# Kernel optimization log

Hardware: AMD Instinct MI355X
Metric: run time of the kernel (lower is better)

## Reference

```python
import jax, jax.numpy as jnp
import numpy as np

# Mega (Flash-Quad) encoder layer: MultiHeadEMA + moving-average gated chunked attention + ScaleNorm
L, B, D = 2048, 16, 512        # seq_len, batch, embed_dim (fairseq L,B,D layout)
H, Z, NDIM = 1024, 128, 2      # hdim, zdim, EMA ndim
CHUNK = 128                    # Flash-Quad chunk size
MAXPOS = 1024                  # SimpleRelativePositionalBias max positions
EPS = 1e-6                     # ScaleNorm eps


def setup_inputs() -> dict:
    key = jax.random.key(0)
    ks = jax.random.split(key, 16)
    def nrm(k, shape, s=0.02):
        return jax.random.normal(k, shape, jnp.float32) * s
    return dict(
        x=jax.random.normal(ks[0], (L, B, D), jnp.float32),
        # MultiHeadEMA params (bidirectional -> kernel_dim = 2*D)
        ema_delta=nrm(ks[1], (2 * D, NDIM, 1), 1.0),
        ema_alpha=nrm(ks[2], (2 * D, NDIM, 1), 1.0),
        ema_beta=nrm(ks[3], (2 * D, NDIM, 1), 0.02),
        ema_gamma=nrm(ks[4], (2 * D, NDIM), 1.0),
        ema_omega=nrm(ks[5], (D,), 1.0),
        # projections
        Wv=nrm(ks[6], (D, H)), bv=jnp.zeros((H,), jnp.float32),
        Wmx=nrm(ks[7], (D, Z + H + 2 * D)), bmx=jnp.zeros((Z + H + 2 * D,), jnp.float32),
        Wh=nrm(ks[8], (H, D)), bh=jnp.zeros((D,), jnp.float32),
        # per-dim q/k affine (gamma/beta) on shared z
        qk_gamma=nrm(ks[9], (2, Z), 0.1) + 1.0,
        qk_beta=nrm(ks[10], (2, Z), 0.1),
        # simple relative positional bias over chunk length
        rel_pos_bias=nrm(ks[11], (2 * MAXPOS - 1,), 0.02),
        # ScaleNorm scalar
        norm_scalar=jnp.ones((), jnp.float32),
    )


def _ema(x, delta, alpha, beta, gamma, omega):
    """Bidirectional multi-dim damped EMA via FFT convolution. x: (L,B,D) -> (L,B,D)."""
    Lx, Bx, Dx = x.shape
    residual = x * omega
    xt = jnp.transpose(x, (1, 2, 0))                      # B,D,L
    p = jax.nn.sigmoid(delta)                             # 2D,n,1
    q = 1.0 - p * jax.nn.sigmoid(alpha)                   # 2D,n,1 in (0,1)
    vander = jnp.arange(Lx, dtype=jnp.float32)[None, None, :] * jnp.log(q)  # 2D,n,L
    kern = jnp.einsum('dnl,dn->dl', (p * beta) * jnp.exp(vander),
                      gamma * (1.0 / np.sqrt(NDIM)))      # 2D,L
    k1, k2 = kern[:Dx], kern[Dx:]
    # combined causal + anticausal kernel of length 2L-1, input left-padded by L-1
    kc = jnp.pad(k1, ((0, 0), (Lx - 1, 0))) + jnp.pad(k2[:, ::-1], ((0, 0), (0, Lx - 1)))
    xp = jnp.pad(xt, ((0, 0), (0, 0), (Lx - 1, 0)))
    n = 2 * (2 * Lx - 1)
    out = jnp.fft.irfft(jnp.fft.rfft(xp, n=n) * jnp.fft.rfft(kc, n=n), n=n)
    out = out[..., 2 * Lx - 2: 2 * Lx - 2 + Lx]           # B,D,L
    return jax.nn.silu(jnp.transpose(out, (2, 0, 1)) + residual)


def _forward(x, ema_delta, ema_alpha, ema_beta, ema_gamma, ema_omega,
             Wv, bv, Wmx, bmx, Wh, bh, qk_gamma, qk_beta, rel_pos_bias, norm_scalar):
    Lx, Bx, Dx = x.shape
    residual = x
    v = jax.nn.silu(x @ Wv + bv)                          # L,B,H
    mx = _ema(x, ema_delta, ema_alpha, ema_beta, ema_gamma, ema_omega)  # L,B,D
    base = mx @ Wmx + bmx                                 # L,B,D+Z+H+D
    u = jax.nn.sigmoid(base[..., :Dx])                    # update gate
    zr = jax.nn.silu(base[..., Dx:Dx + Z + H])
    hx = base[..., Dx + Z + H:]
    z, r = zr[..., :Z], zr[..., Z:]                       # shared z, reset gate r
    zqk = z[..., None, :] * qk_gamma + qk_beta            # L,B,2,Z
    nc = Lx // CHUNK
    q = jnp.transpose(zqk[..., 0, :], (1, 0, 2)).reshape(Bx, nc, CHUNK, Z)
    k = jnp.transpose(zqk[..., 1, :], (1, 0, 2)).reshape(Bx, nc, CHUNK, Z)
    vc = jnp.transpose(v, (1, 0, 2)).reshape(Bx, nc, CHUNK, H)
    # Toeplitz relative bias: bias[i,j] = rel_pos_bias[MAXPOS-1 + j - i]
    idx = (MAXPOS - 1) + jnp.arange(CHUNK)[None, :] - jnp.arange(CHUNK)[:, None]
    bias = rel_pos_bias[idx]                              # C,C
    qk = jnp.einsum('bnqz,bnkz->bnqk', q * (Z ** -0.5), k) + bias
    attn = jax.nn.softmax(qk, axis=-1)                    # B,nc,C,C
    h = jnp.einsum('bnqk,bnkh->bnqh', attn, vc).reshape(Bx, Lx, H)
    h = jnp.transpose(h, (1, 0, 2))                       # L,B,H
    h = jax.nn.silu(hx + (h * r) @ Wh + bh)               # L,B,D
    out = residual + u * (h - residual)                   # addcmul gated residual
    ms = jnp.mean(out * out, axis=-1, keepdims=True)      # ScaleNorm
    out = norm_scalar * out * jax.lax.rsqrt(ms + EPS)
    return out, attn


def reference(x, ema_delta, ema_alpha, ema_beta, ema_gamma, ema_omega,
              Wv, bv, Wmx, bmx, Wh, bh, qk_gamma, qk_beta, rel_pos_bias, norm_scalar):
    return _forward(x, ema_delta, ema_alpha, ema_beta, ema_gamma, ema_omega,
                    Wv, bv, Wmx, bmx, Wh, bh, qk_gamma, qk_beta, rel_pos_bias, norm_scalar)
```

## Files before the change

### kernel.cpp

```cpp
#include <hip/hip_runtime.h>
#include <math.h>

#define L_DIM 2048
#define B_DIM 16
#define D_DIM 512
#define H_DIM 1024
#define Z_DIM 128
#define NC    16
#define BASE_N 2176
#define ROWS  (L_DIM*B_DIM)
#define NSEG  32
#define SLEN  64
#define CHAINS 8192

typedef unsigned short bf16_t;
typedef __attribute__((ext_vector_type(8))) short short8;
typedef __attribute__((ext_vector_type(4))) float f32x4;

__device__ __forceinline__ float sigmoidf_(float x){ return 1.f/(1.f+__expf(-x)); }
__device__ __forceinline__ float siluf_(float x){ return x/(1.f+__expf(-x)); }
__device__ __forceinline__ float fbits(unsigned int b){ union{unsigned int i; float f;} c; c.i=b; return c.f; }
__device__ __forceinline__ unsigned short f2bf(float f){
  union{float f; unsigned int i;} c; c.f=f;
  unsigned int r = c.i + 0x7FFFu + ((c.i>>16)&1u);
  return (unsigned short)(r>>16);
}
__device__ __forceinline__ float bf2f(unsigned short u){ return fbits(((unsigned int)u)<<16); }

__device__ __forceinline__ void load8(const float* __restrict__ p, float* d){
  float4 a = *(const float4*)p; float4 b = *(const float4*)(p+4);
  d[0]=a.x; d[1]=a.y; d[2]=a.z; d[3]=a.w; d[4]=b.x; d[5]=b.y; d[6]=b.z; d[7]=b.w;
}
__device__ __forceinline__ void load8(const bf16_t* __restrict__ p, float* d){
  uint4 u = *(const uint4*)p;
  d[0]=fbits(u.x<<16); d[1]=fbits(u.x&0xFFFF0000u);
  d[2]=fbits(u.y<<16); d[3]=fbits(u.y&0xFFFF0000u);
  d[4]=fbits(u.z<<16); d[5]=fbits(u.z&0xFFFF0000u);
  d[6]=fbits(u.w<<16); d[7]=fbits(u.w&0xFFFF0000u);
}
__device__ __forceinline__ void store8bf(bf16_t* p, const float* v){
  uint4 s;
  s.x = (unsigned int)f2bf(v[0]) | ((unsigned int)f2bf(v[1])<<16);
  s.y = (unsigned int)f2bf(v[2]) | ((unsigned int)f2bf(v[3])<<16);
  s.z = (unsigned int)f2bf(v[4]) | ((unsigned int)f2bf(v[5])<<16);
  s.w = (unsigned int)f2bf(v[6]) | ((unsigned int)f2bf(v[7])<<16);
  *(uint4*)p = s;
}

__device__ __forceinline__ void glds16(const void* g, void* l) {
  __builtin_amdgcn_global_load_lds(
      (const __attribute__((address_space(1))) unsigned int*)g,
      (__attribute__((address_space(3))) unsigned int*)l, 16, 0, 0);
}

__global__ __launch_bounds__(256) void transpose_all_kernel(
    const float* __restrict__ Wv, const float* __restrict__ Wmx,
    const float* __restrict__ Wh, bf16_t* __restrict__ Wvt,
    bf16_t* __restrict__ Wmxt, bf16_t* __restrict__ Wht)
{
  __shared__ float t[32][33];
  int blk = blockIdx.x;
  const float* W; bf16_t* Wt; int K, N, bx, by;
  if (blk < 512)       { W=Wv;  Wt=Wvt;  K=512;  N=1024; bx=blk&31;  by=blk>>5; }
  else if (blk < 1600) { blk-=512;  W=Wmx; Wt=Wmxt; K=512;  N=2176; bx=blk%68; by=blk/68; }
  else                 { blk-=1600; W=Wh;  Wt=Wht;  K=1024; N=512;  bx=blk&15; by=blk>>4; }
  int lx = threadIdx.x & 31, ly = threadIdx.x >> 5;
  #pragma unroll
  for (int i = 0; i < 32; i += 8)
    t[ly+i][lx] = W[(size_t)(by*32+ly+i)*N + bx*32 + lx];
  __syncthreads();
  #pragma unroll
  for (int i = 0; i < 32; i += 8)
    Wt[(size_t)(bx*32+ly+i)*K + by*32 + lx] = f2bf(t[lx][ly+i]);
}

__global__ __launch_bounds__(256) void ema_carry_kernel(
    const float* __restrict__ x, const float* __restrict__ delta,
    const float* __restrict__ alpha, bf16_t* __restrict__ xb,
    float* __restrict__ carry)
{
  int idx = blockIdx.x*256 + threadIdx.x;
  int d = idx & 511, c = idx & 8191, s = idx >> 13;
  float qf0 = 1.f - sigmoidf_(delta[d*2+0])*sigmoidf_(alpha[d*2+0]);
  float qf1 = 1.f - sigmoidf_(delta[d*2+1])*sigmoidf_(alpha[d*2+1]);
  int dd = d + 512;
  float qb0 = 1.f - sigmoidf_(delta[dd*2+0])*sigmoidf_(alpha[dd*2+0]);
  float qb1 = 1.f - sigmoidf_(delta[dd*2+1])*sigmoidf_(alpha[dd*2+1]);
  size_t off = (size_t)s*SLEN*CHAINS + c;
  float h0=0.f, h1=0.f;
  #pragma unroll
  for (int t = 0; t < SLEN; ++t) {
    size_t a = off + (size_t)t*CHAINS;
    float xv = x[a];
    xb[a] = f2bf(xv);
    h0 = fmaf(qf0, h0, xv); h1 = fmaf(qf1, h1, xv);
  }
  float g0=0.f, g1=0.f;
  #pragma unroll
  for (int t = SLEN-1; t >= 0; --t) {
    float xv = bf2f(xb[off + (size_t)t*CHAINS]);
    g0 = fmaf(qb0, g0, xv); g1 = fmaf(qb1, g1, xv);
  }
  carry[(size_t)s*CHAINS + c]              = h0;
  carry[(size_t)s*CHAINS + c + 262144]     = h1;
  carry[(size_t)s*CHAINS + c + 524288]     = g0;
  carry[(size_t)s*CHAINS + c + 786432]     = g1;
}

__global__ __launch_bounds__(256) void ema_combine_kernel(
    const float* __restrict__ delta, const float* __restrict__ alpha,
    float* __restrict__ carry)
{
  int c = blockIdx.x*256 + threadIdx.x;
  int d = c & 511;
  float qf0 = 1.f - sigmoidf_(delta[d*2+0])*sigmoidf_(alpha[d*2+0]);
  float qf1 = 1.f - sigmoidf_(delta[d*2+1])*sigmoidf_(alpha[d*2+1]);
  int dd = d + 512;
  float qb0 = 1.f - sigmoidf_(delta[dd*2+0])*sigmoidf_(alpha[dd*2+0]);
  float qb1 = 1.f - sigmoidf_(delta[dd*2+1])*sigmoidf_(alpha[dd*2+1]);
  float df0=qf0, df1=qf1, db0=qb0, db1=qb1;
  #pragma unroll
  for (int i = 0; i < 6; ++i) { df0*=df0; df1*=df1; db0*=db0; db1*=db1; }
  float h0=0.f, h1=0.f;
  for (int s = 0; s < NSEG; ++s) {
    size_t a = (size_t)s*CHAINS + c;
    float t0 = carry[a], t1 = carry[a+262144];
    carry[a] = h0; carry[a+262144] = h1;
    h0 = fmaf(df0, h0, t0); h1 = fmaf(df1, h1, t1);
  }
  float g0=0.f, g1=0.f;
  for (int s = NSEG-1; s >= 0; --s) {
    size_t a = (size_t)s*CHAINS + c;
    float t0 = carry[a+524288], t1 = carry[a+786432];
    carry[a+524288] = g0; carry[a+786432] = g1;
    g0 = fmaf(db0, g0, t0); g1 = fmaf(db1, g1, t1);
  }
}

__global__ __launch_bounds__(256) void ema_apply_kernel(
    const bf16_t* __restrict__ xb, const float* __restrict__ delta,
    const float* __restrict__ alpha, const float* __restrict__ beta,
    const float* __restrict__ gamma, const float* __restrict__ omega,
    const float* __restrict__ carry, bf16_t* __restrict__ mx)
{
  int idx = blockIdx.x*256 + threadIdx.x;
  int d = idx & 511, c = idx & 8191, s = idx >> 13;
  const float rs = 0.70710678118654752f;
  float pf0 = sigmoidf_(delta[d*2+0]), pf1 = sigmoidf_(delta[d*2+1]);
  float qf0 = 1.f - pf0*sigmoidf_(alpha[d*2+0]);
  float qf1 = 1.f - pf1*sigmoidf_(alpha[d*2+1]);
  float cf0 = pf0*beta[d*2+0]*gamma[d*2+0]*rs;
  float cf1 = pf1*beta[d*2+1]*gamma[d*2+1]*rs;
  int dd = d + 512;
  float pb0 = sigmoidf_(delta[dd*2+0]), pb1 = sigmoidf_(delta[dd*2+1]);
  float qb0 = 1.f - pb0*sigmoidf_(alpha[dd*2+0]);
  float qb1 = 1.f - pb1*sigmoidf_(alpha[dd*2+1]);
  float cb0 = pb0*beta[dd*2+0]*gamma[dd*2+0]*rs;
  float cb1 = pb1*beta[dd*2+1]*gamma[dd*2+1]*rs;
  float om = omega[d];
  size_t off = (size_t)s*SLEN*CHAINS + c;
  float h0 = carry[(size_t)s*CHAINS + c];
  float h1 = carry[(size_t)s*CHAINS + c + 262144];
  float yv[SLEN];
  #pragma unroll
  for (int t = 0; t < SLEN; ++t) {
    float xv = bf2f(xb[off + (size_t)t*CHAINS]);
    h0 = fmaf(qf0, h0, xv); h1 = fmaf(qf1, h1, xv);
    yv[t] = fmaf(cf0, h0, cf1*h1);
  }
  float g0 = carry[(size_t)s*CHAINS + c + 524288];
  float g1 = carry[(size_t)s*CHAINS + c + 786432];
  #pragma unroll
  for (int t = SLEN-1; t >= 0; --t) {
    size_t a = off + (size_t)t*CHAINS;
    float xv = bf2f(xb[a]);
    g0 = fmaf(qb0, g0, xv); g1 = fmaf(qb1, g1, xv);
    float sv = yv[t] + fmaf(cb0, g0, cb1*g1) + xv*om;
    mx[a] = f2bf(siluf_(sv));
  }
}

#define GEMM_PROLOG(Aptr, Bptr, Kdim)                                        \
  int tid = threadIdx.x;                                                     \
  int wave = tid >> 6, lane = tid & 63;                                      \
  int lrow = lane >> 3, lchunk = ((lane & 7) - lrow) & 7;                    \
  const bf16_t* Ag = (Aptr) + (size_t)(wave*32 + lrow)*(Kdim) + lchunk*8;    \
  const bf16_t* Bg = (Bptr) + (size_t)(wave*32 + lrow)*(Kdim) + lchunk*8;    \
  int wm = wave >> 1, wn = wave & 1;                                         \
  int fr = lane & 15, fq = lane >> 4;                                        \
  f32x4 acc[4][4];                                                           \
  _Pragma("unroll") for (int i = 0; i < 4; ++i)                              \
    _Pragma("unroll") for (int j = 0; j < 4; ++j)                            \
      acc[i][j] = (f32x4){0.f,0.f,0.f,0.f};

#define GEMM_KLOOP(Kdim)                                                     \
  for (int k0 = 0; k0 < (Kdim); k0 += 64) {                                  \
    __syncthreads();                                                         \
    _Pragma("unroll") for (int j = 0; j < 4; ++j) {                          \
      glds16(Ag + (size_t)j*8*(Kdim) + k0, As + (wave*32 + j*8)*64);         \
      glds16(Bg + (size_t)j*8*(Kdim) + k0, Bs + (wave*32 + j*8)*64);         \
    }                                                                        \
    __syncthreads();                                                         \
    _Pragma("unroll") for (int kk = 0; kk < 2; ++kk) {                       \
      short8 af[4], bfr[4];                                                  \
      _Pragma("unroll") for (int mi = 0; mi < 4; ++mi) {                     \
        int R = wm*64 + mi*16 + fr;                                          \
        af[mi] = *(const short8*)&As[R*64 + (((kk<<2)+fq+R)&7)*8];           \
      }                                                                      \
      _Pragma("unroll") for (int ni = 0; ni < 4; ++ni) {                     \
        int R = wn*64 + ni*16 + fr;                                          \
        bfr[ni] = *(const short8*)&Bs[R*64 + (((kk<<2)+fq+R)&7)*8];          \
      }                                                                      \
      _Pragma("unroll") for (int mi = 0; mi < 4; ++mi)                       \
        _Pragma("unroll") for (int ni = 0; ni < 4; ++ni)                     \
          acc[mi][ni] = __builtin_amdgcn_mfma_f32_16x16x32_bf16(             \
              af[mi], bfr[ni], acc[mi][ni], 0, 0, 0);                        \
    }                                                                        \
  }

__global__ __launch_bounds__(256) void mfma_gemm_kernel(
    const bf16_t* __restrict__ A, const bf16_t* __restrict__ Bt,
    const float* __restrict__ bias, const bf16_t* __restrict__ Add, int addLd,
    bf16_t* __restrict__ C, int N, int K, int nT, int act)
{
  __shared__ __align__(16) char smem[34816];
  bf16_t* As = (bf16_t*)smem;
  bf16_t* Bs = (bf16_t*)(smem + 16384);
  bf16_t* Cs = (bf16_t*)smem;
  int flat = blockIdx.x;
  int xcd = flat & 7, g = flat >> 3;
  int mT8 = (int)(gridDim.x / (unsigned)nT) >> 3;
  int mt = xcd*mT8 + g / nT;
  int nt = g % nT;
  int m0 = mt*128, n0 = nt*128;
  GEMM_PROLOG(A + (size_t)m0*K, Bt + (size_t)n0*K, K)
  GEMM_KLOOP(K)
  __syncthreads();
  #pragma unroll
  for (int ni = 0; ni < 4; ++ni) {
    int cl = wn*64 + ni*16 + fr;
    int gn = n0 + cl;
    float bv = bias[gn];
    #pragma unroll
    for (int mi = 0; mi < 4; ++mi) {
      #pragma unroll
      for (int r = 0; r < 4; ++r) {
        int ml = wm*64 + mi*16 + fq*4 + r;
        float val = acc[mi][ni][r] + bv;
        if (Add) val += bf2f(Add[(size_t)(m0+ml)*addLd + gn]);
        if (act == 1) val = siluf_(val);
        Cs[ml*136 + cl] = f2bf(val);
      }
    }
  }
  __syncthreads();
  int row = tid >> 1, c0 = (tid & 1)*64;
  #pragma unroll
  for (int q = 0; q < 8; ++q)
    *(uint4*)(C + (size_t)(m0+row)*N + n0 + c0 + q*8) =
        *(const uint4*)&Cs[row*136 + c0 + q*8];
}

__global__ __launch_bounds__(256) void mfma_gemm_v_kernel(
    const bf16_t* __restrict__ A, const bf16_t* __restrict__ Bt,
    const float* __restrict__ bias, bf16_t* __restrict__ vt, int nT, int K)
{
  __shared__ __align__(16) char smem[34816];
  bf16_t* As = (bf16_t*)smem;
  bf16_t* Bs = (bf16_t*)(smem + 16384);
  bf16_t* Cs = (bf16_t*)smem;
  int flat = blockIdx.x;
  int xcd = flat & 7, g = flat >> 3;
  int mT8 = (int)(gridDim.x / (unsigned)nT) >> 3;
  int mt = xcd*mT8 + g / nT;
  int nt = g % nT;
  int m0 = mt*128, n0 = nt*128;
  GEMM_PROLOG(A + (size_t)m0*K, Bt + (size_t)n0*K, K)
  GEMM_KLOOP(K)
  __syncthreads();
  #pragma unroll
  for (int ni = 0; ni < 4; ++ni) {
    int cl = wn*64 + ni*16 + fr;
    float bv = bias[n0 + cl];
    #pragma unroll
    for (int mi = 0; mi < 4; ++mi) {
      #pragma unroll
      for (int r = 0; r < 4; ++r) {
        int ml = wm*64 + mi*16 + fq*4 + r;
        Cs[ml*136 + cl] = f2bf(siluf_(acc[mi][ni][r] + bv));
      }
    }
  }
  __syncthreads();
  int b = tid >> 4, h0l = (tid & 15)*8;
  int nchunk = mt >> 4, kbase = (mt & 15)*8;
  #pragma unroll
  for (int j = 0; j < 8; ++j) {
    int hl = h0l + j;
    uint4 s;
    s.x = (unsigned int)Cs[(0*16 + b)*136 + hl] |
          ((unsigned int)Cs[(1*16 + b)*136 + hl] << 16);
    s.y = (unsigned int)Cs[(2*16 + b)*136 + hl] |
          ((unsigned int)Cs[(3*16 + b)*136 + hl] << 16);
    s.z = (unsigned int)Cs[(4*16 + b)*136 + hl] |
          ((unsigned int)Cs[(5*16 + b)*136 + hl] << 16);
    s.w = (unsigned int)Cs[(6*16 + b)*136 + hl] |
          ((unsigned int)Cs[(7*16 + b)*136 + hl] << 16);
    *(uint4*)&vt[((size_t)(b*NC + nchunk)*H_DIM + n0 + hl)*128 + kbase] = s;
  }
}

__global__ __launch_bounds__(256) void attn_scores_mfma_kernel(
    const bf16_t* __restrict__ base, const float* __restrict__ qkg,
    const float* __restrict__ qkb, const float* __restrict__ rpb,
    float* __restrict__ attn_out, bf16_t* __restrict__ p_bf)
{
  __shared__ bf16_t qs[128*136];
  __shared__ bf16_t ks[128*136];
  int blk = blockIdx.x;
  int b = blk >> 4, n = blk & 15;
  int tid = threadIdx.x;
  {
    int r = tid >> 1, z0 = (tid & 1)*64;
    size_t rowoff = ((size_t)((n*128 + r)*B_DIM + b))*BASE_N + 512 + z0;
    #pragma unroll
    for (int cchunk = 0; cchunk < 8; ++cchunk) {
      float t8[8], qv[8], kv[8];
      load8(base + rowoff + cchunk*8, t8);
      #pragma unroll
      for (int j = 0; j < 8; ++j) {
        int z = z0 + cchunk*8 + j;
        float zs = siluf_(t8[j]);
        qv[j] = fmaf(zs, qkg[z],     qkb[z]);
        kv[j] = fmaf(zs, qkg[128+z], qkb[128+z]);
      }
      store8bf(&qs[r*136 + z0 + cchunk*8], qv);
      store8bf(&ks[r*136 + z0 + cchunk*8], kv);
    }
  }
  __syncthreads();
  int wave = tid >> 6, lane = tid & 63;
  int fr = lane & 15, fq = lane >> 4;
  f32x4 acc[2][8];
  #pragma unroll
  for (int i = 0; i < 2; ++i)
    #pragma unroll
    for (int j = 0; j < 8; ++j)
      acc[i][j] = (f32x4){0.f,0.f,0.f,0.f};
  #pragma unroll
  for (int kk = 0; kk < 4; ++kk) {
    short8 af[2], bfr[8];
    #pragma unroll
    for (int mi = 0; mi < 2; ++mi)
      af[mi] = *(const short8*)&qs[(wave*32 + mi*16 + fr)*136 + kk*32 + fq*8];
    #pragma unroll
    for (int ni = 0; ni < 8; ++ni)
      bfr[ni] = *(const short8*)&ks[(ni*16 + fr)*136 + kk*32 + fq*8];
    #pragma unroll
    for (int mi = 0; mi < 2; ++mi)
      #pragma unroll
      for (int ni = 0; ni < 8; ++ni)
        acc[mi][ni] = __builtin_amdgcn_mfma_f32_16x16x32_bf16(
            af[mi], bfr[ni], acc[mi][ni], 0, 0, 0);
  }
  const float scale = 0.08838834764831845f;
  float mrow[2][4], srow[2][4];
  #pragma unroll
  for (int mi = 0; mi < 2; ++mi)
    #pragma unroll
    for (int r = 0; r < 4; ++r) mrow[mi][r] = -1e30f;
  #pragma unroll
  for (int mi = 0; mi < 2; ++mi)
    #pragma unroll
    for (int ni = 0; ni < 8; ++ni)
      #pragma unroll
      for (int r = 0; r < 4; ++r) {
        int i = wave*32 + mi*16 + fq*4 + r;
        int j = ni*16 + fr;
        float v = fmaf(acc[mi][ni][r], scale, rpb[1023 + j - i]);
        acc[mi][ni][r] = v;
        mrow[mi][r] = fmaxf(mrow[mi][r], v);
      }
  #pragma unroll
  for (int mi = 0; mi < 2; ++mi)
    #pragma unroll
    for (int r = 0; r < 4; ++r) {
      float m = mrow[mi][r];
      m = fmaxf(m, __shfl_xor(m, 1));
      m = fmaxf(m, __shfl_xor(m, 2));
      m = fmaxf(m, __shfl_xor(m, 4));
      m = fmaxf(m, __shfl_xor(m, 8));
      mrow[mi][r] = m;
      srow[mi][r] = 0.f;
    }
  #pragma unroll
  for (int mi = 0; mi < 2; ++mi)
    #pragma unroll
    for (int ni = 0; ni < 8; ++ni)
      #pragma unroll
      for (int r = 0; r < 4; ++r) {
        float e = __expf(acc[mi][ni][r] - mrow[mi][r]);
        acc[mi][ni][r] = e;
        srow[mi][r] += e;
      }
  #pragma unroll
  for (int mi = 0; mi < 2; ++mi)
    #pragma unroll
    for (int r = 0; r < 4; ++r) {
      float s = srow[mi][r];
      s += __shfl_xor(s, 1);
      s += __shfl_xor(s, 2);
      s += __shfl_xor(s, 4);
      s += __shfl_xor(s, 8);
      srow[mi][r] = 1.f/s;
    }
  #pragma unroll
  for (int mi = 0; mi < 2; ++mi)
    #pragma unroll
    for (int r = 0; r < 4; ++r) {
      int i = wave*32 + mi*16 + fq*4 + r;
      size_t o = ((size_t)blk*128 + i)*128;
      #pragma unroll
      for (int ni = 0; ni < 8; ++ni) {
        float val = acc[mi][ni][r]*srow[mi][r];
        attn_out[o + ni*16 + fr] = val;
        p_bf[o + ni*16 + fr] = f2bf(val);
      }
    }
}

__global__ __launch_bounds__(256) void attn_pv_kernel(
    const bf16_t* __restrict__ p_bf, const bf16_t* __restrict__ vt,
    const bf16_t* __restrict__ base, bf16_t* __restrict__ hr)
{
  __shared__ __align__(16) char smem[34816];
  bf16_t* As = (bf16_t*)smem;
  bf16_t* Bs = (bf16_t*)(smem + 16384);
  bf16_t* Cs = (bf16_t*)smem;
  int blk = blockIdx.x >> 3, ht = blockIdx.x & 7;
  int b = blk >> 4, n = blk & 15;
  const int K = 128;
  GEMM_PROLOG(p_bf + (size_t)blk*(128*128),
              vt + ((size_t)blk*H_DIM + ht*128)*128, K)
  GEMM_KLOOP(K)
  __syncthreads();
  #pragma unroll
  for (int ni = 0; ni < 4; ++ni) {
    int cl = wn*64 + ni*16 + fr;
    int hg = ht*128 + cl;
    #pragma unroll
    for (int mi = 0; mi < 4; ++mi) {
      #pragma unroll
      for (int r = 0; r < 4; ++r) {
        int ml = wm*64 + mi*16 + fq*4 + r;
        size_t rowg = (size_t)((n*128 + ml)*B_DIM + b);
        float rg = bf2f(base[rowg*BASE_N + 640 + hg]);
        Cs[ml*136 + cl] = f2bf(acc[mi][ni][r]*siluf_(rg));
      }
    }
  }
  __syncthreads();
  int row = tid >> 1, c0 = (tid & 1)*64;
  size_t rowg = (size_t)((n*128 + row)*B_DIM + b);
  #pragma unroll
  for (int q = 0; q < 8; ++q)
    *(uint4*)(hr + rowg*H_DIM + ht*128 + c0 + q*8) =
        *(const uint4*)&Cs[row*136 + c0 + q*8];
}

__global__ __launch_bounds__(64) void final_kernel(
    const float* __restrict__ x, const bf16_t* __restrict__ h2,
    const bf16_t* __restrict__ base, const float* __restrict__ ns,
    float* __restrict__ out)
{
  int row = blockIdx.x;
  int t = threadIdx.x;
  size_t ro = (size_t)row*D_DIM + t*8;
  float xv[8]; load8(x + ro, xv);
  float hv[8]; load8(h2 + ro, hv);
  float uv[8]; load8(base + (size_t)row*BASE_N + t*8, uv);
  float o[8];
  float ss = 0.f;
  #pragma unroll
  for (int i = 0; i < 8; ++i) {
    float u = sigmoidf_(uv[i]);
    o[i] = xv[i] + u*(hv[i] - xv[i]);
    ss += o[i]*o[i];
  }
  #pragma unroll
  for (int m = 1; m < 64; m <<= 1) ss += __shfl_xor(ss, m);
  float inv = rsqrtf(ss*(1.f/(float)D_DIM) + 1e-6f) * ns[0];
  float4 r0, r1;
  r0.x = o[0]*inv; r0.y = o[1]*inv; r0.z = o[2]*inv; r0.w = o[3]*inv;
  r1.x = o[4]*inv; r1.y = o[5]*inv; r1.z = o[6]*inv; r1.w = o[7]*inv;
  *(float4*)(out + ro) = r0;
  *(float4*)(out + ro + 4) = r1;
}

extern "C" void kernel_launch(void* const* d_in, const int* in_sizes, int n_in,
                              void* d_out, int out_size, void* d_ws, size_t ws_size,
                              hipStream_t stream)
{
  const float* x     = (const float*)d_in[0];
  const float* delta = (const float*)d_in[1];
  const float* alpha = (const float*)d_in[2];
  const float* beta  = (const float*)d_in[3];
  const float* gamma = (const float*)d_in[4];
  const float* omega = (const float*)d_in[5];
  const float* Wv    = (const float*)d_in[6];
  const float* bv    = (const float*)d_in[7];
  const float* Wmx   = (const float*)d_in[8];
  const float* bmx   = (const float*)d_in[9];
  const float* Wh    = (const float*)d_in[10];
  const float* bh    = (const float*)d_in[11];
  const float* qkg   = (const float*)d_in[12];
  const float* qkb   = (const float*)d_in[13];
  const float* rpb   = (const float*)d_in[14];
  const float* ns    = (const float*)d_in[15];

  float* out  = (float*)d_out;
  float* attn = out + (size_t)ROWS*D_DIM;

  char* outb = (char*)d_out;
  bf16_t* x_bf  = (bf16_t*)outb;
  bf16_t* p_bf  = (bf16_t*)outb;
  bf16_t* Wv_t  = (bf16_t*)(outb + 33554432ull);
  bf16_t* Wmx_t = (bf16_t*)(outb + 34603008ull);
  bf16_t* Wh_t  = (bf16_t*)(outb + 36831232ull);

  const size_t WS_NEED = 310378496ull;
  if (ws_size < WS_NEED) return;
  char* wsb = (char*)d_ws;
  bf16_t* mx_bf   = (bf16_t*)(wsb);
  bf16_t* vt      = (bf16_t*)(wsb + 33554432ull);
  bf16_t* base_bf = (bf16_t*)(wsb + 100663296ull);
  bf16_t* hr_bf   = (bf16_t*)(wsb + 243269632ull);
  float*  carry   = (float*)(wsb + 100663296ull);
  bf16_t* h2_bf   = mx_bf;

  transpose_all_kernel<<<2112, 256, 0, stream>>>(Wv, Wmx, Wh, Wv_t, Wmx_t, Wh_t);
  ema_carry_kernel<<<1024, 256, 0, stream>>>(x, delta, alpha, x_bf, carry);
  ema_combine_kernel<<<32, 256, 0, stream>>>(delta, alpha, carry);
  ema_apply_kernel<<<1024, 256, 0, stream>>>(x_bf, delta, alpha, beta, gamma,
                                             omega, carry, mx_bf);
  mfma_gemm_v_kernel<<<2048, 256, 0, stream>>>(x_bf, Wv_t, bv, vt, 8, D_DIM);
  mfma_gemm_kernel<<<4352, 256, 0, stream>>>(
      mx_bf, Wmx_t, bmx, nullptr, 0, base_bf, BASE_N, D_DIM, 17, 0);
  attn_scores_mfma_kernel<<<B_DIM*NC, 256, 0, stream>>>(
      base_bf, qkg, qkb, rpb, attn, p_bf);
  attn_pv_kernel<<<2048, 256, 0, stream>>>(p_bf, vt, base_bf, hr_bf);
  mfma_gemm_kernel<<<1024, 256, 0, stream>>>(
      hr_bf, Wh_t, bh, base_bf + 1664, BASE_N, h2_bf, D_DIM, H_DIM, 4, 1);
  final_kernel<<<ROWS, 64, 0, stream>>>(x, h2_bf, base_bf, ns, out);
}
```

Baseline: 631.0 us.

## Double-buffer GEMM LDS tiles with K=32 stages; batch final rows; keep EMA inputs in registers

After: 649.0 us. +2.9%, slower.

```diff
diff --git a/kernel.cpp b/kernel.cpp
--- a/kernel.cpp
+++ b/kernel.cpp
@@ -87,18 +87,21 @@
   float qb0 = 1.f - sigmoidf_(delta[dd*2+0])*sigmoidf_(alpha[dd*2+0]);
   float qb1 = 1.f - sigmoidf_(delta[dd*2+1])*sigmoidf_(alpha[dd*2+1]);
   size_t off = (size_t)s*SLEN*CHAINS + c;
+  float xr[SLEN];
   float h0=0.f, h1=0.f;
   #pragma unroll
   for (int t = 0; t < SLEN; ++t) {
     size_t a = off + (size_t)t*CHAINS;
     float xv = x[a];
-    xb[a] = f2bf(xv);
+    unsigned short xv16 = f2bf(xv);
+    xb[a] = xv16;
+    xr[t] = bf2f(xv16);
     h0 = fmaf(qf0, h0, xv); h1 = fmaf(qf1, h1, xv);
   }
   float g0=0.f, g1=0.f;
   #pragma unroll
   for (int t = SLEN-1; t >= 0; --t) {
-    float xv = bf2f(xb[off + (size_t)t*CHAINS]);
+    float xv = xr[t];
     g0 = fmaf(qb0, g0, xv); g1 = fmaf(qb1, g1, xv);
   }
   carry[(size_t)s*CHAINS + c]              = h0;
@@ -180,42 +183,56 @@
   }
 }
 
+#define GEMM_SMEM                                                            \
+  __shared__ __align__(16) char smem[34816];                                 \
+  bf16_t* As0 = (bf16_t*)smem;                                               \
+  bf16_t* Bs0 = (bf16_t*)(smem + 8192);                                      \
+  bf16_t* As1 = (bf16_t*)(smem + 16384);                                     \
+  bf16_t* Bs1 = (bf16_t*)(smem + 24576);                                     \
+  bf16_t* Cs  = (bf16_t*)smem;
+
 #define GEMM_PROLOG(Aptr, Bptr, Kdim)                                        \
   int tid = threadIdx.x;                                                     \
   int wave = tid >> 6, lane = tid & 63;                                      \
-  int lrow = lane >> 3, lchunk = ((lane & 7) - lrow) & 7;                    \
+  int lrow = lane >> 2, lchunk = ((lane & 3) - ((lane >> 2) & 3)) & 3;       \
   const bf16_t* Ag = (Aptr) + (size_t)(wave*32 + lrow)*(Kdim) + lchunk*8;    \
   const bf16_t* Bg = (Bptr) + (size_t)(wave*32 + lrow)*(Kdim) + lchunk*8;    \
   int wm = wave >> 1, wn = wave & 1;                                         \
   int fr = lane & 15, fq = lane >> 4;                                        \
+  int slotA = (fq + fr) & 3;                                                 \
   f32x4 acc[4][4];                                                           \
   _Pragma("unroll") for (int i = 0; i < 4; ++i)                              \
     _Pragma("unroll") for (int j = 0; j < 4; ++j)                            \
       acc[i][j] = (f32x4){0.f,0.f,0.f,0.f};
 
+#define GEMM_STAGE(Asd, Bsd, koff, Kdim)                                     \
+  _Pragma("unroll") for (int j = 0; j < 2; ++j) {                            \
+    glds16(Ag + (size_t)j*16*(Kdim) + (koff), (Asd) + (wave*32 + j*16)*32);  \
+    glds16(Bg + (size_t)j*16*(Kdim) + (koff), (Bsd) + (wave*32 + j*16)*32);  \
+  }
+
 #define GEMM_KLOOP(Kdim)                                                     \
-  for (int k0 = 0; k0 < (Kdim); k0 += 64) {                                  \
-    __syncthreads();                                                         \
-    _Pragma("unroll") for (int j = 0; j < 4; ++j) {                          \
-      glds16(Ag + (size_t)j*8*(Kdim) + k0, As + (wave*32 + j*8)*64);         \
-      glds16(Bg + (size_t)j*8*(Kdim) + k0, Bs + (wave*32 + j*8)*64);         \
+  GEMM_STAGE(As0, Bs0, 0, Kdim)                                              \
+  for (int k0 = 0, cur = 0; k0 < (Kdim); k0 += 32, cur ^= 1) {               \
+    __syncthreads();            \
+    bf16_t* Asc = cur ? As1 : As0;  bf16_t* Bsc = cur ? Bs1 : Bs0;           \
+    bf16_t* Asn = cur ? As0 : As1;  bf16_t* Bsn = cur ? Bs0 : Bs1;           \
+    if (k0 + 32 < (Kdim)) {                                                  \
+      GEMM_STAGE(Asn, Bsn, k0 + 32, Kdim)                                    \
     }                                                                        \
-    __syncthreads();                                                         \
-    _Pragma("unroll") for (int kk = 0; kk < 2; ++kk) {                       \
-      short8 af[4], bfr[4];                                                  \
-      _Pragma("unroll") for (int mi = 0; mi < 4; ++mi) {                     \
-        int R = wm*64 + mi*16 + fr;                                          \
-        af[mi] = *(const short8*)&As[R*64 + (((kk<<2)+fq+R)&7)*8];           \
-      }                                                                      \
-      _Pragma("unroll") for (int ni = 0; ni < 4; ++ni) {                     \
-        int R = wn*64 + ni*16 + fr;                                          \
-        bfr[ni] = *(const short8*)&Bs[R*64 + (((kk<<2)+fq+R)&7)*8];          \
-      }                                                                      \
-      _Pragma("unroll") for (int mi = 0; mi < 4; ++mi)                       \
-        _Pragma("unroll") for (int ni = 0; ni < 4; ++ni)                     \
-          acc[mi][ni] = __builtin_amdgcn_mfma_f32_16x16x32_bf16(             \
-              af[mi], bfr[ni], acc[mi][ni], 0, 0, 0);                        \
+    short8 af[4], bfr[4];                                                    \
+    _Pragma("unroll") for (int mi = 0; mi < 4; ++mi) {                       \
+      int R = wm*64 + mi*16 + fr;                                            \
+      af[mi] = *(const short8*)&Asc[R*32 + slotA*8];                         \
     }                                                                        \
+    _Pragma("unroll") for (int ni = 0; ni < 4; ++ni) {                       \
+      int R = wn*64 + ni*16 + fr;                                            \
+      bfr[ni] = *(const short8*)&Bsc[R*32 + slotA*8];                        \
+    }                                                                        \
+    _Pragma("unroll") for (int mi = 0; mi < 4; ++mi)                         \
+      _Pragma("unroll") for (int ni = 0; ni < 4; ++ni)                       \
+        acc[mi][ni] = __builtin_amdgcn_mfma_f32_16x16x32_bf16(               \
+            af[mi], bfr[ni], acc[mi][ni], 0, 0, 0);                          \
   }
 
 __global__ __launch_bounds__(256) void mfma_gemm_kernel(
@@ -223,10 +240,7 @@
     const float* __restrict__ bias, const bf16_t* __restrict__ Add, int addLd,
     bf16_t* __restrict__ C, int N, int K, int nT, int act)
 {
-  __shared__ __align__(16) char smem[34816];
-  bf16_t* As = (bf16_t*)smem;
-  bf16_t* Bs = (bf16_t*)(smem + 16384);
-  bf16_t* Cs = (bf16_t*)smem;
+  GEMM_SMEM
   int flat = blockIdx.x;
   int xcd = flat & 7, g = flat >> 3;
   int mT8 = (int)(gridDim.x / (unsigned)nT) >> 3;
@@ -265,10 +279,7 @@
     const bf16_t* __restrict__ A, const bf16_t* __restrict__ Bt,
     const float* __restrict__ bias, bf16_t* __restrict__ vt, int nT, int K)
 {
-  __shared__ __align__(16) char smem[34816];
-  bf16_t* As = (bf16_t*)smem;
-  bf16_t* Bs = (bf16_t*)(smem + 16384);
-  bf16_t* Cs = (bf16_t*)smem;
+  GEMM_SMEM
   int flat = blockIdx.x;
   int xcd = flat & 7, g = flat >> 3;
   int mT8 = (int)(gridDim.x / (unsigned)nT) >> 3;
@@ -433,10 +444,7 @@
     const bf16_t* __restrict__ p_bf, const bf16_t* __restrict__ vt,
     const bf16_t* __restrict__ base, bf16_t* __restrict__ hr)
 {
-  __shared__ __align__(16) char smem[34816];
-  bf16_t* As = (bf16_t*)smem;
-  bf16_t* Bs = (bf16_t*)(smem + 16384);
-  bf16_t* Cs = (bf16_t*)smem;
+  GEMM_SMEM
   int blk = blockIdx.x >> 3, ht = blockIdx.x & 7;
   int b = blk >> 4, n = blk & 15;
   const int K = 128;
@@ -468,13 +476,13 @@
         *(const uint4*)&Cs[row*136 + c0 + q*8];
 }
 
-__global__ __launch_bounds__(64) void final_kernel(
+__global__ __launch_bounds__(256) void final_kernel(
     const float* __restrict__ x, const bf16_t* __restrict__ h2,
     const bf16_t* __restrict__ base, const float* __restrict__ ns,
     float* __restrict__ out)
 {
-  int row = blockIdx.x;
-  int t = threadIdx.x;
+  int row = blockIdx.x*4 + (threadIdx.x >> 6);
+  int t = threadIdx.x & 63;
   size_t ro = (size_t)row*D_DIM + t*8;
   float xv[8]; load8(x + ro, xv);
   float hv[8]; load8(h2 + ro, hv);
@@ -551,5 +559,5 @@
   attn_pv_kernel<<<2048, 256, 0, stream>>>(p_bf, vt, base_bf, hr_bf);
   mfma_gemm_kernel<<<1024, 256, 0, stream>>>(
       hr_bf, Wh_t, bh, base_bf + 1664, BASE_N, h2_bf, D_DIM, H_DIM, 4, 1);
-  final_kernel<<<ROWS, 64, 0, stream>>>(x, h2_bf, base_bf, ns, out);
-}
+  final_kernel<<<ROWS/4, 256, 0, stream>>>(x, h2_bf, base_bf, ns, out);
+}
```
